# Performance work log

Hardware: AMD Instinct MI355X
Metric: run time of the kernel (lower is better)

## Reference

```python
import jax, jax.numpy as jnp
import numpy as np

B, N, D, S, ITERS = 64, 2048, 256, 8, 3
SCALE = D ** -0.5
EPS_LN = 1e-5

def _ln(x, g, b):
    m = jnp.mean(x, axis=-1, keepdims=True)
    v = jnp.var(x, axis=-1, keepdims=True)
    return (x - m) / jnp.sqrt(v + EPS_LN) * g + b

def setup_inputs() -> dict:
    key = jax.random.key(0)
    ks = jax.random.split(key, 20)
    s = D ** -0.5
    f32 = jnp.float32
    return dict(
        x=jax.random.normal(ks[0], (B, N, D), f32),
        noise=jax.random.normal(ks[1], (B, S, D), f32),
        slots_mu=jax.random.normal(ks[2], (1, 1, D), f32),
        slots_sigma=jax.random.normal(ks[3], (1, 1, D), f32),
        Wq=jax.random.normal(ks[4], (D, D), f32) * s, bq=jnp.zeros((D,), f32),
        Wk=jax.random.normal(ks[5], (D, D), f32) * s, bk=jnp.zeros((D,), f32),
        Wv=jax.random.normal(ks[6], (D, D), f32) * s, bv=jnp.zeros((D,), f32),
        W_ih=jax.random.normal(ks[7], (3 * D, D), f32) * s, b_ih=jnp.zeros((3 * D,), f32),
        W_hh=jax.random.normal(ks[8], (3 * D, D), f32) * s, b_hh=jnp.zeros((3 * D,), f32),
        W1=jax.random.normal(ks[9], (D, D), f32) * s, b1=jnp.zeros((D,), f32),
        W2=jax.random.normal(ks[10], (D, D), f32) * s, b2=jnp.zeros((D,), f32),
        g_in=jnp.ones((D,), f32), be_in=jnp.zeros((D,), f32),
        g_sl=jnp.ones((D,), f32), be_sl=jnp.zeros((D,), f32),
        g_ff=jnp.ones((D,), f32), be_ff=jnp.zeros((D,), f32),
    )

def reference(x, noise, slots_mu, slots_sigma, Wq, bq, Wk, bk, Wv, bv,
              W_ih, b_ih, W_hh, b_hh, W1, b1, W2, b2,
              g_in, be_in, g_sl, be_sl, g_ff, be_ff):
    # slot init: mu + softplus(sigma) * noise  -> [B,S,D]
    slots = slots_mu + jax.nn.softplus(slots_sigma) * noise
    xn = _ln(x, g_in, be_in)
    k = xn @ Wk.T + bk  # [B,N,D]
    v = xn @ Wv.T + bv
    for _ in range(ITERS):
        prev = slots
        q = _ln(slots, g_sl, be_sl) @ Wq.T + bq  # [B,S,D]
        logits = jnp.einsum('bsd,bnd->bsn', q, k) * SCALE
        attn = jax.nn.softmax(logits, axis=-1) + 1e-8  # softmax over inputs, as in source
        attn = attn / jnp.sum(attn, axis=-1, keepdims=True)
        updates = jnp.einsum('bsn,bnd->bsd', attn, v)
        # GRUCell(input=updates, hidden=prev); torch gate order r,z,n
        gi = updates @ W_ih.T + b_ih
        gh = prev @ W_hh.T + b_hh
        ir, iz, i_n = jnp.split(gi, 3, axis=-1)
        hr, hz, h_n = jnp.split(gh, 3, axis=-1)
        r = jax.nn.sigmoid(ir + hr)
        z = jax.nn.sigmoid(iz + hz)
        n = jnp.tanh(i_n + r * h_n)
        slots = (1.0 - z) * n + z * prev
        # residual MLP
        h = jax.nn.relu(_ln(slots, g_ff, be_ff) @ W1.T + b1)
        slots = slots + (h @ W2.T + b2)
    return slots
```

## Files before the change

kernel.cpp:

```cpp
#include <hip/hip_runtime.h>
#include <cstddef>


#define BB 64
#define NN 2048
#define DD 256
#define NCH 8
#define CHK 256
#define NITER 3

typedef unsigned short u16;
typedef unsigned int u32;
typedef _Float16 h2 __attribute__((ext_vector_type(2)));
typedef _Float16 h4 __attribute__((ext_vector_type(4)));

#if defined(__has_builtin)
#if __has_builtin(__builtin_amdgcn_fdot2)
#define HAS_FDOT2 1
#endif
#endif

#ifdef HAS_FDOT2
#define FDOT2(a,b,c) __builtin_amdgcn_fdot2((a),(b),(c),false)
#else
#define FDOT2(a,b,c) fmaf((float)(a).y,(float)(b).y, fmaf((float)(a).x,(float)(b).x,(c)))
#endif

__device__ __forceinline__ h2 u2h2(u32 v){ union{u32 u; h2 h;} c; c.u=v; return c.h; }

__global__ __launch_bounds__(256) void kA(const float* __restrict__ x, const float* __restrict__ g_in,
                                          const float* __restrict__ be_in, u16* __restrict__ xn,
                                          const float* __restrict__ noise, const float* __restrict__ mu,
                                          const float* __restrict__ sig, float* __restrict__ S,
                                          const float* __restrict__ Wq, const float* __restrict__ Wk,
                                          const float* __restrict__ bq, const float* __restrict__ Wih,
                                          const float* __restrict__ Wv, const float* __restrict__ bv,
                                          const float* __restrict__ bih,
                                          float* __restrict__ Wqk, float* __restrict__ bqk,
                                          float* __restrict__ Wihv, float* __restrict__ bihv){
  __shared__ float col[256];
  const int t = threadIdx.x;
  const int blk = blockIdx.x;
  if(blk < 256){
    col[t] = Wq[t*256 + blk];
    __syncthreads();
    float acc = 0.f;
    #pragma unroll 4
    for(int j=0;j<256;j++) acc += col[j]*Wk[j*256+t];
    Wqk[blk*256+t] = acc * 0.0625f;
  } else if(blk < 1024){
    int c = blk - 256;
    col[t] = Wih[c*256+t];
    __syncthreads();
    float acc = 0.f;
    #pragma unroll 4
    for(int j=0;j<256;j++) acc += col[j]*Wv[j*256+t];
    Wihv[(size_t)c*256+t] = acc;
  } else if(blk < 1536){
    int i = (blk-1024)*256 + t;
    float sg = sig[t];
    float sp = fmaxf(sg, 0.f) + log1pf(expf(-fabsf(sg)));
    S[i] = mu[t] + sp * noise[i];
  } else if(blk == 1536){
    float acc = 0.f;
    for(int j=0;j<256;j++) acc += bq[j]*Wk[j*256+t];
    bqk[t] = acc * 0.0625f;
  } else if(blk == 1537){
    for(int c=t;c<768;c+=256){
      float acc = 0.f;
      for(int j=0;j<256;j++) acc += Wih[c*256+j]*bv[j];
      bihv[c] = acc + bih[c];
    }
  } else {
    int wave = t>>6, lane = t&63;
    size_t row = (size_t)(blk-1538)*4 + wave;
    float4 v = *(const float4*)(x + row*256 + lane*4);
    float s1 = v.x+v.y+v.z+v.w;
    float s2 = v.x*v.x + v.y*v.y + v.z*v.z + v.w*v.w;
    #pragma unroll
    for(int off=1; off<64; off<<=1){ s1 += __shfl_xor(s1,off); s2 += __shfl_xor(s2,off); }
    float m = s1*(1.f/256.f);
    float var = s2*(1.f/256.f) - m*m;
    float rs = rsqrtf(var + 1e-5f);
    float4 gg = *(const float4*)(g_in + lane*4);
    float4 bb = *(const float4*)(be_in + lane*4);
    union { h4 h; ushort4 s4; } pk;
    pk.h[0] = (_Float16)((v.x-m)*rs*gg.x + bb.x);
    pk.h[1] = (_Float16)((v.y-m)*rs*gg.y + bb.y);
    pk.h[2] = (_Float16)((v.z-m)*rs*gg.z + bb.z);
    pk.h[3] = (_Float16)((v.w-m)*rs*gg.w + bb.w);
    *(ushort4*)(xn + row*256 + lane*4) = pk.s4;
  }
}

__global__ __launch_bounds__(256) void kB(const float* __restrict__ Wihv, const float* __restrict__ Whh,
                                          const float* __restrict__ W1, const float* __restrict__ W2,
                                          float* __restrict__ WihvT, float* __restrict__ WhhT,
                                          float* __restrict__ W1T, float* __restrict__ W2T,
                                          const float* __restrict__ S0, const float* __restrict__ g_sl,
                                          const float* __restrict__ be_sl, const float* __restrict__ Wqk,
                                          const float* __restrict__ bqk, float* __restrict__ Qq){
  __shared__ float tile[64][65];
  __shared__ float lnA[8][256];
  const int blk = blockIdx.x, t = threadIdx.x;
  if(blk < 128){
    const float* src; float* dst; int R, C, tb;
    if(blk < 48){ src=Wihv; dst=WihvT; R=768; C=256; tb=blk; }
    else if(blk < 96){ src=Whh; dst=WhhT; R=768; C=256; tb=blk-48; }
    else if(blk < 112){ src=W1; dst=W1T; R=256; C=256; tb=blk-96; }
    else { src=W2; dst=W2T; R=256; C=256; tb=blk-112; }
    const int tilesC = C/64;
    const int r0 = (tb/tilesC)*64, c0 = (tb%tilesC)*64;
    const int x = t&63, y = t>>6;
    #pragma unroll
    for(int k=0;k<16;k++) tile[y*16+k][x] = src[(size_t)(r0+y*16+k)*C + c0+x];
    __syncthreads();
    #pragma unroll
    for(int k=0;k<16;k++) dst[(size_t)(c0+y*16+k)*R + r0+x] = tile[x][y*16+k];
    return;
  }
  const int w = t>>6, l = t&63;
  const int r0 = (blk-128)*8;
  #pragma unroll
  for(int rr=0; rr<2; rr++){
    int r = w*2 + rr;
    float4 v = *(const float4*)(S0 + (size_t)(r0+r)*256 + l*4);
    float s1 = v.x+v.y+v.z+v.w;
    float s2 = v.x*v.x+v.y*v.y+v.z*v.z+v.w*v.w;
    #pragma unroll
    for(int off=1; off<64; off<<=1){ s1 += __shfl_xor(s1,off); s2 += __shfl_xor(s2,off); }
    float m = s1*(1.f/256.f);
    float var = s2*(1.f/256.f) - m*m;
    float rs = rsqrtf(var + 1e-5f);
    float4 gg = *(const float4*)(g_sl + l*4);
    float4 bb = *(const float4*)(be_sl + l*4);
    float4 o;
    o.x=(v.x-m)*rs*gg.x+bb.x; o.y=(v.y-m)*rs*gg.y+bb.y;
    o.z=(v.z-m)*rs*gg.z+bb.z; o.w=(v.w-m)*rs*gg.w+bb.w;
    *(float4*)(&lnA[r][l*4]) = o;
  }
  __syncthreads();
  const int c4 = l*4;
  float acc[2][4] = {};
  #pragma unroll 2
  for(int k=0;k<256;k++){
    float4 wv = *(const float4*)(Wqk + (size_t)k*256 + c4);
    float a0 = lnA[2*w][k], a1 = lnA[2*w+1][k];
    acc[0][0]+=a0*wv.x; acc[0][1]+=a0*wv.y; acc[0][2]+=a0*wv.z; acc[0][3]+=a0*wv.w;
    acc[1][0]+=a1*wv.x; acc[1][1]+=a1*wv.y; acc[1][2]+=a1*wv.z; acc[1][3]+=a1*wv.w;
  }
  float4 bq4 = *(const float4*)(bqk + c4);
  #pragma unroll
  for(int rr=0; rr<2; rr++){
    float4 o;
    o.x=acc[rr][0]+bq4.x; o.y=acc[rr][1]+bq4.y; o.z=acc[rr][2]+bq4.z; o.w=acc[rr][3]+bq4.w;
    *(float4*)(Qq + (size_t)(r0+2*w+rr)*256 + c4) = o;
  }
}

__global__ __launch_bounds__(256) void k_attn(const float* __restrict__ Qq, const u16* __restrict__ xn,
                                              float* __restrict__ mP, float* __restrict__ lP,
                                              float* __restrict__ aP){
  __shared__ h2 qsh[4][128];
  __shared__ float plT[4][256];
  __shared__ float mS[4], lS[4];
  __shared__ float4 red[4][4][64];
  const int b = blockIdx.x, c = blockIdx.y, z = blockIdx.z, t = threadIdx.x;
  const int w = t>>6, l = t&63;
  for(int i=t; i<512; i+=256){
    int s = i>>7, p = i&127;
    float a = Qq[b*2048 + z*1024 + s*256 + 2*p];
    float bq = Qq[b*2048 + z*1024 + s*256 + 2*p + 1];
    h2 hv; hv.x = (_Float16)a; hv.y = (_Float16)bq;
    qsh[s][p] = hv;
  }
  __syncthreads();
  const uint4* xr = (const uint4*)(xn + ((size_t)(b*NN) + (size_t)c*CHK + t)*DD);
  float lg[4]={0,0,0,0};
  #pragma unroll 4
  for(int d8=0; d8<32; ++d8){
    uint4 u = xr[d8];
    h2 xa=u2h2(u.x), xb=u2h2(u.y), xc=u2h2(u.z), xd=u2h2(u.w);
    #pragma unroll
    for(int s=0;s<4;s++){
      const h2* qp = &qsh[s][d8*4];
      float acc = lg[s];
      acc = FDOT2(xa, qp[0], acc);
      acc = FDOT2(xb, qp[1], acc);
      acc = FDOT2(xc, qp[2], acc);
      acc = FDOT2(xd, qp[3], acc);
      lg[s] = acc;
    }
  }
  #pragma unroll
  for(int s=0;s<4;s++) plT[s][t] = lg[s];
  __syncthreads();
  {
    float mx = -1e30f;
    #pragma unroll
    for(int k=0;k<4;k++) mx = fmaxf(mx, plT[w][l + 64*k]);
    #pragma unroll
    for(int off=1; off<64; off<<=1) mx = fmaxf(mx, __shfl_xor(mx, off));
    if(l==0) mS[w] = mx;
  }
  __syncthreads();
  #pragma unroll
  for(int s=0;s<4;s++) plT[s][t] = __expf(lg[s] - mS[s]);
  __syncthreads();
  {
    float sm = 0.f;
    #pragma unroll
    for(int k=0;k<4;k++) sm += plT[w][l + 64*k];
    #pragma unroll
    for(int off=1; off<64; off<<=1) sm += __shfl_xor(sm, off);
    if(l==0) lS[w] = sm;
  }
  __syncthreads();
  {
    float4 acc4[4] = {};
    const u16* base = xn + ((size_t)(b*NN) + (size_t)c*CHK)*DD;
    #pragma unroll 8
    for(int j=0;j<64;++j){
      int nl = w + 4*j;
      uint2 u = *(const uint2*)(base + (size_t)nl*DD + l*4);
      h2 ha=u2h2(u.x), hb=u2h2(u.y);
      float x0=(float)ha.x, x1=(float)ha.y, x2=(float)hb.x, x3=(float)hb.y;
      float p0=plT[0][nl], p1=plT[1][nl], p2=plT[2][nl], p3=plT[3][nl];
      acc4[0].x += p0*x0; acc4[0].y += p0*x1; acc4[0].z += p0*x2; acc4[0].w += p0*x3;
      acc4[1].x += p1*x0; acc4[1].y += p1*x1; acc4[1].z += p1*x2; acc4[1].w += p1*x3;
      acc4[2].x += p2*x0; acc4[2].y += p2*x1; acc4[2].z += p2*x2; acc4[2].w += p2*x3;
      acc4[3].x += p3*x0; acc4[3].y += p3*x1; acc4[3].z += p3*x2; acc4[3].w += p3*x3;
    }
    #pragma unroll
    for(int s=0;s<4;s++) red[w][s][l] = acc4[s];
  }
  __syncthreads();
  const size_t pb = (size_t)(b*NCH + c)*8 + z*4;
  {
    int s = t>>6, ll = t&63;
    float4 r0=red[0][s][ll], r1=red[1][s][ll], r2=red[2][s][ll], r3=red[3][s][ll];
    float4 o;
    o.x=r0.x+r1.x+r2.x+r3.x; o.y=r0.y+r1.y+r2.y+r3.y;
    o.z=r0.z+r1.z+r2.z+r3.z; o.w=r0.w+r1.w+r2.w+r3.w;
    *(float4*)(aP + (pb + s)*256 + ll*4) = o;
  }
  if(t<4){ mP[pb+t] = mS[t]; lP[pb+t] = lS[t]; }
}

__global__ __launch_bounds__(512) void k_post(const float* __restrict__ mP, const float* __restrict__ lP,
                                              const float* __restrict__ aP, const float* __restrict__ WihvT,
                                              const float* __restrict__ bihv, const float* __restrict__ WhhT,
                                              const float* __restrict__ bhh, const float* __restrict__ Sc,
                                              const float* __restrict__ g_ff, const float* __restrict__ be_ff,
                                              const float* __restrict__ W1T, const float* __restrict__ b1,
                                              const float* __restrict__ W2T, const float* __restrict__ b2,
                                              const float* __restrict__ g_sl, const float* __restrict__ be_sl,
                                              const float* __restrict__ Wqk, const float* __restrict__ bqk,
                                              float* __restrict__ Sout, float* __restrict__ Qq, int writeQ){
  __shared__ float Ut[256], Sp[256], Gt[2][768];
  __shared__ float Row[256], Ht[256], Snew[256], Lq[256], Hp[2][256];
  __shared__ float red2[2][4];
  const int t = threadIdx.x;
  const int c = t&255, h = t>>8, w4 = (t>>6)&3, l = t&63;
  const int r = blockIdx.x;
  const int b = r>>3, s = r&7;
  if(t < 256){
    const float* mpb = mP + b*64 + s;
    const float* lpb = lP + b*64 + s;
    float M = -1e30f;
    #pragma unroll
    for(int c8=0;c8<8;c8++) M = fmaxf(M, mpb[c8*8]);
    float wc[8]; float L = 0.f;
    #pragma unroll
    for(int c8=0;c8<8;c8++){ wc[c8] = __expf(mpb[c8*8] - M); L += lpb[c8*8]*wc[c8]; }
    float inv = 1.f/L;
    size_t base = ((size_t)b*64 + s)*256 + c;
    float u = 0.f;
    #pragma unroll
    for(int c8=0;c8<8;c8++) u += wc[c8]*aP[base + (size_t)c8*2048];
    Ut[c] = u*inv;
    Sp[c] = Sc[(size_t)r*256 + c];
  }
  __syncthreads();
  if(t < 384){
    const int mat = t/192, q4 = (t - mat*192)*4;
    const float* WT = mat ? WhhT : WihvT;
    const float* bb = mat ? bhh : bihv;
    const float* A  = mat ? Sp : Ut;
    float4 acc = *(const float4*)(bb + q4);
    const float* wp = WT + q4;
    #pragma unroll 8
    for(int d=0; d<256; ++d){
      float4 wv = *(const float4*)(wp + (size_t)d*768);
      float a = A[d];
      acc.x += a*wv.x; acc.y += a*wv.y; acc.z += a*wv.z; acc.w += a*wv.w;
    }
    *(float4*)(&Gt[mat][q4]) = acc;
  }
  __syncthreads();
  if(t < 256){
    float gir = Gt[0][c], giz = Gt[0][256+c], gin = Gt[0][512+c];
    float ghr = Gt[1][c], ghz = Gt[1][256+c], ghn = Gt[1][512+c];
    float rr = 1.f/(1.f + __expf(-(gir+ghr)));
    float zz = 1.f/(1.f + __expf(-(giz+ghz)));
    float nn = tanhf(gin + rr*ghn);
    float sp = (1.f-zz)*nn + zz*Sp[c];
    Ut[c] = sp;
    float s1 = sp, s2 = sp*sp;
    #pragma unroll
    for(int off=1; off<64; off<<=1){ s1 += __shfl_xor(s1,off); s2 += __shfl_xor(s2,off); }
    if(l==0){ red2[0][w4] = s1; red2[1][w4] = s2; }
  }
  __syncthreads();
  if(t < 256){
    float t1 = red2[0][0]+red2[0][1]+red2[0][2]+red2[0][3];
    float t2 = red2[1][0]+red2[1][1]+red2[1][2]+red2[1][3];
    float m = t1*(1.f/256.f);
    float var = t2*(1.f/256.f) - m*m;
    float rs = rsqrtf(var + 1e-5f);
    Row[c] = (Ut[c]-m)*rs*g_ff[c] + be_ff[c];
  }
  __syncthreads();
  {
    const float* w1 = W1T + (size_t)h*128*256 + c;
    float acc = h ? 0.f : b1[c];
    const float* rw = &Row[h*128];
    #pragma unroll 8
    for(int d=0; d<128; ++d) acc += rw[d]*w1[(size_t)d*256];
    Hp[h][c] = acc;
  }
  __syncthreads();
  if(t < 256) Ht[c] = fmaxf(Hp[0][c]+Hp[1][c], 0.f);
  __syncthreads();
  {
    const float* w2 = W2T + (size_t)h*128*256 + c;
    float acc = h ? 0.f : b2[c];
    const float* hw = &Ht[h*128];
    #pragma unroll 8
    for(int d=0; d<128; ++d) acc += hw[d]*w2[(size_t)d*256];
    Hp[h][c] = acc;
  }
  __syncthreads();
  if(t < 256){
    float sn = Hp[0][c]+Hp[1][c] + Ut[c];
    Sout[(size_t)r*256 + c] = sn;
    Snew[c] = sn;
  }
  if(writeQ){
    __syncthreads();
    if(t < 256){
      float sn = Snew[c];
      float s1 = sn, s2 = sn*sn;
      #pragma unroll
      for(int off=1; off<64; off<<=1){ s1 += __shfl_xor(s1,off); s2 += __shfl_xor(s2,off); }
      if(l==0){ red2[0][w4] = s1; red2[1][w4] = s2; }
    }
    __syncthreads();
    if(t < 256){
      float t1 = red2[0][0]+red2[0][1]+red2[0][2]+red2[0][3];
      float t2 = red2[1][0]+red2[1][1]+red2[1][2]+red2[1][3];
      float m = t1*(1.f/256.f);
      float var = t2*(1.f/256.f) - m*m;
      float rs = rsqrtf(var + 1e-5f);
      Lq[c] = (Snew[c]-m)*rs*g_sl[c] + be_sl[c];
    }
    __syncthreads();
    {
      const float* wq = Wqk + (size_t)h*128*256 + c;
      float acc = h ? 0.f : bqk[c];
      const float* lw = &Lq[h*128];
      #pragma unroll 8
      for(int d=0; d<128; ++d) acc += lw[d]*wq[(size_t)d*256];
      Hp[h][c] = acc;
    }
    __syncthreads();
    if(t < 256) Qq[(size_t)r*256 + c] = Hp[0][c]+Hp[1][c];
  }
}

extern "C" void kernel_launch(void* const* d_in, const int* in_sizes, int n_in,
                              void* d_out, int out_size, void* d_ws, size_t ws_size,
                              hipStream_t stream){
  const float* x    = (const float*)d_in[0];
  const float* noise= (const float*)d_in[1];
  const float* mu   = (const float*)d_in[2];
  const float* sig  = (const float*)d_in[3];
  const float* Wq   = (const float*)d_in[4];
  const float* bq   = (const float*)d_in[5];
  const float* Wk   = (const float*)d_in[6];
  const float* Wv   = (const float*)d_in[8];
  const float* bv   = (const float*)d_in[9];
  const float* W_ih = (const float*)d_in[10];
  const float* b_ih = (const float*)d_in[11];
  const float* W_hh = (const float*)d_in[12];
  const float* b_hh = (const float*)d_in[13];
  const float* W1m  = (const float*)d_in[14];
  const float* b1v  = (const float*)d_in[15];
  const float* W2m  = (const float*)d_in[16];
  const float* b2v  = (const float*)d_in[17];
  const float* g_in = (const float*)d_in[18];
  const float* be_in= (const float*)d_in[19];
  const float* g_sl = (const float*)d_in[20];
  const float* be_sl= (const float*)d_in[21];
  const float* g_ff = (const float*)d_in[22];
  const float* be_ff= (const float*)d_in[23];

  char* p = (char*)d_ws;
  auto alloc = [&](size_t bytes)->char*{ char* q = p; p += (bytes + 255) & ~(size_t)255; return q; };
  u16*   xn    = (u16*)  alloc((size_t)BB*NN*DD*2);
  float* Wqk   = (float*)alloc(256*256*4);
  float* bqk   = (float*)alloc(256*4);
  float* Wihv  = (float*)alloc((size_t)768*256*4);
  float* WihvT = (float*)alloc((size_t)256*768*4);
  float* bihv  = (float*)alloc(768*4);
  float* WhhT  = (float*)alloc((size_t)256*768*4);
  float* W1T   = (float*)alloc(256*256*4);
  float* W2T   = (float*)alloc(256*256*4);
  float* S0    = (float*)alloc(512*256*4);
  float* S1    = (float*)alloc(512*256*4);
  float* Qq    = (float*)alloc(512*256*4);
  float* mP    = (float*)alloc(64*NCH*8*4);
  float* lP    = (float*)alloc(64*NCH*8*4);
  float* aP    = (float*)alloc((size_t)64*NCH*8*256*4);
  if((size_t)(p - (char*)d_ws) > ws_size) return;

  kA<<<34306, 256, 0, stream>>>(x, g_in, be_in, xn, noise, mu, sig, S0,
                                Wq, Wk, bq, W_ih, Wv, bv, b_ih, Wqk, bqk, Wihv, bihv);
  kB<<<192, 256, 0, stream>>>(Wihv, W_hh, W1m, W2m, WihvT, WhhT, W1T, W2T,
                              S0, g_sl, be_sl, Wqk, bqk, Qq);

  float* Sin = S0;
  float* Sping[2] = { S1, S0 };
  for(int it=0; it<NITER; ++it){
    float* Sout = (it==NITER-1) ? (float*)d_out : Sping[it&1];
    k_attn<<<dim3(64, NCH, 2), 256, 0, stream>>>(Qq, xn, mP, lP, aP);
    k_post<<<512, 512, 0, stream>>>(mP, lP, aP, WihvT, bihv, WhhT, b_hh, Sin, g_ff, be_ff,
                                    W1T, b1v, W2T, b2v, g_sl, be_sl, Wqk, bqk,
                                    Sout, Qq, (it<NITER-1) ? 1 : 0);
    Sin = Sout;
  }
}
```

Baseline: 330.8 us.

## Stage xn chunk in LDS and process all 8 slots per block

k_attn previously launched two blocks per (batch, chunk), one per half of the slots, so each 256x256 fp16 chunk of xn was read from global memory twice (logits and weighted sum) by two blocks. Now one 512-thread block copies the chunk once into padded shared memory (pitch 264) and handles all 8 slots. Each wave computes one slot's weighted sum over all 256 rows, which removes the cross-wave reduction buffer. The cost is about 132KB of LDS per block, which limits occupancy to one block per CU, and only 512 blocks are launched.

```diff
diff --git a/kernel.cpp b/kernel.cpp
--- a/kernel.cpp
+++ b/kernel.cpp
@@ -8,6 +8,7 @@
 #define NCH 8
 #define CHK 256
 #define NITER 3
+#define XPITCH 264
 
 typedef unsigned short u16;
 typedef unsigned int u32;
@@ -158,42 +159,54 @@
   }
 }
 
-__global__ __launch_bounds__(256) void k_attn(const float* __restrict__ Qq, const u16* __restrict__ xn,
+__global__ __launch_bounds__(512) void k_attn(const float* __restrict__ Qq, const u16* __restrict__ xn,
                                               float* __restrict__ mP, float* __restrict__ lP,
                                               float* __restrict__ aP){
-  __shared__ h2 qsh[4][128];
-  __shared__ float plT[4][256];
-  __shared__ float mS[4], lS[4];
-  __shared__ float4 red[4][4][64];
-  const int b = blockIdx.x, c = blockIdx.y, z = blockIdx.z, t = threadIdx.x;
+  __shared__ __align__(16) u16 xs[256*XPITCH];
+  __shared__ h2 qs[8][128];
+  __shared__ float plT[8][256];
+  __shared__ float mS[8], lS[8];
+  const int b = blockIdx.x, c = blockIdx.y, t = threadIdx.x;
   const int w = t>>6, l = t&63;
-  for(int i=t; i<512; i+=256){
+  {
+    const uint4* xg4 = (const uint4*)(xn + ((size_t)b*NN + (size_t)c*CHK)*DD);
+    #pragma unroll
+    for(int k=0;k<16;k++){
+      int idx = t + 512*k;
+      int n = idx>>5, j = idx&31;
+      *(uint4*)(xs + (size_t)n*XPITCH + j*8) = xg4[idx];
+    }
+  }
+  for(int i=t; i<1024; i+=512){
     int s = i>>7, p = i&127;
-    float a = Qq[b*2048 + z*1024 + s*256 + 2*p];
-    float bq = Qq[b*2048 + z*1024 + s*256 + 2*p + 1];
+    float a = Qq[b*2048 + s*256 + 2*p];
+    float bq = Qq[b*2048 + s*256 + 2*p + 1];
     h2 hv; hv.x = (_Float16)a; hv.y = (_Float16)bq;
-    qsh[s][p] = hv;
-  }
-  __syncthreads();
-  const uint4* xr = (const uint4*)(xn + ((size_t)(b*NN) + (size_t)c*CHK + t)*DD);
+    qs[s][p] = hv;
+  }
+  __syncthreads();
+  const int n = t & 255, sg = t >> 8;
   float lg[4]={0,0,0,0};
-  #pragma unroll 4
-  for(int d8=0; d8<32; ++d8){
-    uint4 u = xr[d8];
-    h2 xa=u2h2(u.x), xb=u2h2(u.y), xc=u2h2(u.z), xd=u2h2(u.w);
-    #pragma unroll
-    for(int s=0;s<4;s++){
-      const h2* qp = &qsh[s][d8*4];
-      float acc = lg[s];
-      acc = FDOT2(xa, qp[0], acc);
-      acc = FDOT2(xb, qp[1], acc);
-      acc = FDOT2(xc, qp[2], acc);
-      acc = FDOT2(xd, qp[3], acc);
-      lg[s] = acc;
-    }
-  }
-  #pragma unroll
-  for(int s=0;s<4;s++) plT[s][t] = lg[s];
+  {
+    const u16* xr = xs + (size_t)n*XPITCH;
+    #pragma unroll 4
+    for(int d8=0; d8<32; ++d8){
+      uint4 u = *(const uint4*)(xr + d8*8);
+      h2 xa=u2h2(u.x), xb=u2h2(u.y), xc=u2h2(u.z), xd=u2h2(u.w);
+      #pragma unroll
+      for(int k=0;k<4;k++){
+        const h2* qp = &qs[sg*4+k][d8*4];
+        float acc = lg[k];
+        acc = FDOT2(xa, qp[0], acc);
+        acc = FDOT2(xb, qp[1], acc);
+        acc = FDOT2(xc, qp[2], acc);
+        acc = FDOT2(xd, qp[3], acc);
+        lg[k] = acc;
+      }
+    }
+    #pragma unroll
+    for(int k=0;k<4;k++) plT[sg*4+k][n] = lg[k];
+  }
   __syncthreads();
   {
     float mx = -1e30f;
@@ -205,7 +218,7 @@
   }
   __syncthreads();
   #pragma unroll
-  for(int s=0;s<4;s++) plT[s][t] = __expf(lg[s] - mS[s]);
+  for(int k=0;k<4;k++) plT[sg*4+k][n] = __expf(lg[k] - mS[sg*4+k]);
   __syncthreads();
   {
     float sm = 0.f;
@@ -216,35 +229,21 @@
     if(l==0) lS[w] = sm;
   }
   __syncthreads();
-  {
-    float4 acc4[4] = {};
-    const u16* base = xn + ((size_t)(b*NN) + (size_t)c*CHK)*DD;
+  const size_t pb = (size_t)(b*NCH + c)*8;
+  {
+    float4 a4 = {0.f,0.f,0.f,0.f};
+    const u16* xq = xs + 4*l;
     #pragma unroll 8
-    for(int j=0;j<64;++j){
-      int nl = w + 4*j;
-      uint2 u = *(const uint2*)(base + (size_t)nl*DD + l*4);
+    for(int nn=0; nn<256; ++nn){
+      uint2 u = *(const uint2*)(xq + (size_t)nn*XPITCH);
       h2 ha=u2h2(u.x), hb=u2h2(u.y);
-      float x0=(float)ha.x, x1=(float)ha.y, x2=(float)hb.x, x3=(float)hb.y;
-      float p0=plT[0][nl], p1=plT[1][nl], p2=plT[2][nl], p3=plT[3][nl];
-      acc4[0].x += p0*x0; acc4[0].y += p0*x1; acc4[0].z += p0*x2; acc4[0].w += p0*x3;
-      acc4[1].x += p1*x0; acc4[1].y += p1*x1; acc4[1].z += p1*x2; acc4[1].w += p1*x3;
-      acc4[2].x += p2*x0; acc4[2].y += p2*x1; acc4[2].z += p2*x2; acc4[2].w += p2*x3;
-      acc4[3].x += p3*x0; acc4[3].y += p3*x1; acc4[3].z += p3*x2; acc4[3].w += p3*x3;
-    }
-    #pragma unroll
-    for(int s=0;s<4;s++) red[w][s][l] = acc4[s];
-  }
-  __syncthreads();
-  const size_t pb = (size_t)(b*NCH + c)*8 + z*4;
-  {
-    int s = t>>6, ll = t&63;
-    float4 r0=red[0][s][ll], r1=red[1][s][ll], r2=red[2][s][ll], r3=red[3][s][ll];
-    float4 o;
-    o.x=r0.x+r1.x+r2.x+r3.x; o.y=r0.y+r1.y+r2.y+r3.y;
-    o.z=r0.z+r1.z+r2.z+r3.z; o.w=r0.w+r1.w+r2.w+r3.w;
-    *(float4*)(aP + (pb + s)*256 + ll*4) = o;
-  }
-  if(t<4){ mP[pb+t] = mS[t]; lP[pb+t] = lS[t]; }
+      float p = plT[w][nn];
+      a4.x += p*(float)ha.x; a4.y += p*(float)ha.y;
+      a4.z += p*(float)hb.x; a4.w += p*(float)hb.y;
+    }
+    *(float4*)(aP + (pb + w)*256 + l*4) = a4;
+  }
+  if(t<8){ mP[pb+t] = mS[t]; lP[pb+t] = lS[t]; }
 }
 
 __global__ __launch_bounds__(512) void k_post(const float* __restrict__ mP, const float* __restrict__ lP,
@@ -433,7 +432,7 @@
   float* Sping[2] = { S1, S0 };
   for(int it=0; it<NITER; ++it){
     float* Sout = (it==NITER-1) ? (float*)d_out : Sping[it&1];
-    k_attn<<<dim3(64, NCH, 2), 256, 0, stream>>>(Qq, xn, mP, lP, aP);
+    k_attn<<<dim3(64, NCH), 512, 0, stream>>>(Qq, xn, mP, lP, aP);
     k_post<<<512, 512, 0, stream>>>(mP, lP, aP, WihvT, bihv, WhhT, b_hh, Sin, g_ff, be_ff,
                                     W1T, b1v, W2T, b2v, g_sl, be_sl, Wqk, bqk,
                                     Sout, Qq, (it<NITER-1) ? 1 : 0);
```

Result: no change. 328.0 us (-0.8%).
